# Optimization experiments

Measured on AMD Instinct MI355X. Metric: run time of the kernel, lower is better.

Reference implementation:

```python
import jax, jax.numpy as jnp
import numpy as np
from functools import partial

C = 10   # number of regular-repr fields
G = 4    # C4 rotation group order
EPS = 1e-5


def _lift_kernel(w):
    """Lifting (trivial->regular) P4 kernel. w: [C, Cin, k, k] ->
    full kernel [C*G, Cin, k, k] with output channel layout (field, orientation)."""
    ks = [jnp.rot90(w, r, axes=(-2, -1)) for r in range(G)]  # each [C,Cin,k,k]
    k = jnp.stack(ks, axis=1)                                 # [C,G,Cin,k,k]
    return k.reshape(w.shape[0] * G, w.shape[1], w.shape[2], w.shape[3])


def _gconv_kernel(w):
    """Regular->regular P4 kernel. w: [Cout, Cin, G, k, k] (indexed by relative
    input orientation) -> full kernel [Cout*G, Cin*G, k, k].
    K[co*G+r, ci*G+s] = rot90(w[co, ci, (s-r) mod G], r)."""
    Cout, Cin, _, k1, k2 = w.shape
    ks = []
    for r in range(G):
        wr = jnp.roll(w, shift=r, axis=2)             # wr[..., s, :, :] = w[..., (s-r)%G]
        wr = jnp.rot90(wr, r, axes=(-2, -1))          # rotate spatially by r*90deg
        ks.append(wr)
    k = jnp.stack(ks, axis=1)                          # [Cout, G, Cin, G, k, k]
    return k.reshape(Cout * G, Cin * G, k1, k2)


def _conv(x, k, pad):
    return jax.lax.conv_general_dilated(
        x, k, window_strides=(1, 1), padding=pad,
        dimension_numbers=('NCHW', 'OIHW', 'NCHW'))


def _bn_relu(x, gamma, beta):
    """InnerBatchNorm (stats shared over the G orientations of each field) + ReLU."""
    B, CG, H, W = x.shape
    xr = x.reshape(B, C, G, H, W)
    m = xr.mean(axis=(0, 2, 3, 4), keepdims=True)
    v = xr.var(axis=(0, 2, 3, 4), keepdims=True)
    g = gamma[None, :, None, None, None]
    b = beta[None, :, None, None, None]
    y = (xr - m) * jax.lax.rsqrt(v + EPS) * g + b
    return jnp.maximum(y.reshape(B, CG, H, W), 0.0)


def _maxpool2(x):
    return jax.lax.reduce_window(x, -jnp.inf, jax.lax.max,
                                 (1, 1, 2, 2), (1, 1, 2, 2), 'VALID')


def setup_inputs() -> dict:
    key = jax.random.key(0)
    ks = jax.random.split(key, 20)
    B = 1024
    x = jax.random.normal(ks[0], (B, 1, 28, 28), dtype=jnp.float32)
    w1 = jax.random.normal(ks[1], (C, 1, 3, 3), dtype=jnp.float32) * 0.3
    w2 = jax.random.normal(ks[2], (C, C, G, 3, 3), dtype=jnp.float32) * 0.1
    w3 = jax.random.normal(ks[3], (C, C, G, 3, 3), dtype=jnp.float32) * 0.1
    w4 = jax.random.normal(ks[4], (C, C, G, 3, 3), dtype=jnp.float32) * 0.1
    w5 = jax.random.normal(ks[5], (C, C, G, 3, 3), dtype=jnp.float32) * 0.1
    w6 = jax.random.normal(ks[6], (C, C, G, 3, 3), dtype=jnp.float32) * 0.1
    w7 = jax.random.normal(ks[7], (C, C, G, 4, 4), dtype=jnp.float32) * 0.1
    g1 = jnp.ones((C,), jnp.float32) + 0.1 * jax.random.normal(ks[8], (C,))
    b1 = 0.1 * jax.random.normal(ks[9], (C,))
    g2 = jnp.ones((C,), jnp.float32) + 0.1 * jax.random.normal(ks[10], (C,))
    b2 = 0.1 * jax.random.normal(ks[11], (C,))
    gs = jnp.ones((C,), jnp.float32) + 0.1 * jax.random.normal(ks[12], (C,))
    bs = 0.1 * jax.random.normal(ks[13], (C,))
    wfc = jax.random.normal(ks[14], (10, C * 11 * 11), dtype=jnp.float32) * 0.05
    bfc = jnp.zeros((10,), jnp.float32)
    return dict(x=x, w1=w1, w2=w2, w3=w3, w4=w4, w5=w5, w6=w6, w7=w7,
                g1=g1, b1=b1, g2=g2, b2=b2, gs=gs, bs=bs, wfc=wfc, bfc=bfc)


PAD1 = [(1, 1), (1, 1)]
PAD0 = [(0, 0), (0, 0)]


def reference(x, w1, w2, w3, w4, w5, w6, w7, g1, b1, g2, b2, gs, bs, wfc, bfc):
    # block1: lifting P4 conv 3x3 pad1 + InnerBN + ReLU  -> [B, 40, 28, 28]
    h = _bn_relu(_conv(x, _lift_kernel(w1), PAD1), g1, b1)
    # block2: P4 conv + BN + ReLU + 2x2 max pool         -> [B, 40, 14, 14]
    h = _maxpool2(_bn_relu(_conv(h, _gconv_kernel(w2), PAD1), g2, b2))
    # blocks 3-6: P4 conv + shared BN/ReLU               -> [B, 40, 14, 14]
    for w in (w3, w4, w5, w6):
        h = _bn_relu(_conv(h, _gconv_kernel(w), PAD1), gs, bs)
    # block7: P4 conv 4x4 pad0 + shared BN/ReLU          -> [B, 40, 11, 11]
    h = _bn_relu(_conv(h, _gconv_kernel(w7), PAD0), gs, bs)
    # group pooling: max over the G orientations of each field -> [B, 10, 11, 11]
    B = h.shape[0]
    h = h.reshape(B, C, G, 11, 11).max(axis=2)
    # fc
    return h.reshape(B, -1) @ wfc.T + bfc
```

## Files before the change

### kernel.cpp

```cpp
#include <hip/hip_runtime.h>

#define EPSV 1e-5f
#define INV28 (1.f / 3211264.f)
#define INV14 (1.f / 802816.f)
#define INV11 (1.f / 495616.f)

typedef _Float16 v8h __attribute__((ext_vector_type(8)));
typedef _Float16 v4h __attribute__((ext_vector_type(4)));
typedef float v4f __attribute__((ext_vector_type(4)));

__device__ __forceinline__ int rotsrc(int r, int dy, int dx, int K) {
  int sy, sx;
  if (r == 0)      { sy = dy;       sx = dx; }
  else if (r == 1) { sy = dx;       sx = K - 1 - dy; }
  else if (r == 2) { sy = K - 1 - dy; sx = K - 1 - dx; }
  else             { sy = K - 1 - dx; sx = dy; }
  return sy * K + sx;
}

__device__ __forceinline__ float gw_val(const float* __restrict__ w, int oc, int g,
                                        int j, int KS) {
  int tap = g / 5, cig = g % 5, ci = cig * 8 + j;
  int co = oc >> 2, r = oc & 3, cin = ci >> 2, s = ci & 3;
  int srel = (s - r) & 3;
  return w[((co * 10 + cin) * 4 + srel) * (KS * KS) + rotsrc(r, tap / KS, tap % KS, KS)];
}

__device__ __forceinline__ float stat8a(const float* __restrict__ p, int i) {
  float v = 0.f;
#pragma unroll
  for (int c = 0; c < 8; ++c)
    v += __hip_atomic_load(&p[c * 32 + i], __ATOMIC_RELAXED, __HIP_MEMORY_SCOPE_AGENT);
  return v;
}

__global__ void prep_kernel(const float* __restrict__ w1, const float* __restrict__ w2,
                            const float* __restrict__ w3, const float* __restrict__ w4,
                            const float* __restrict__ w5, const float* __restrict__ w6,
                            const float* __restrict__ w7,
                            float* __restrict__ K1, _Float16* __restrict__ Wb,
                            float* __restrict__ stats) {
  int idx = blockIdx.x * blockDim.x + threadIdx.x;
  if (idx < 1792) { stats[idx] = 0.f; return; }
  idx -= 1792;
  if (idx < 360) {
    int tap = idx / 40, oc = idx % 40;
    int c = oc >> 2, r = oc & 3;
    K1[idx] = w1[c * 9 + rotsrc(r, tap / 3, tap % 3, 3)];
    return;
  }
  idx -= 360;
  if (idx < 92160) {
    int l = idx / 18432, r0 = idx % 18432;
    const float* w = (l == 0) ? w2 : (l == 1) ? w3 : (l == 2) ? w4 : (l == 3) ? w5 : w6;
    int mt = r0 / 6144, r1 = r0 % 6144;
    int c = r1 / 512, r2 = r1 % 512;
    int q = r2 / 128, r3 = r2 % 128;
    int ocl = r3 / 8, j = r3 % 8;
    int oc = mt * 16 + ocl, g = c * 4 + q;
    float val = 0.f;
    if (oc < 40 && g < 45) val = gw_val(w, oc, g, j, 3);
    Wb[idx] = (_Float16)val;
    return;
  }
  idx -= 92160;
  if (idx < 30720) {
    int mt = idx / 10240, r1 = idx % 10240;
    int c = r1 / 512, r2 = r1 % 512;
    int q = r2 / 128, r3 = r2 % 128;
    int ocl = r3 / 8, j = r3 % 8;
    int oc = mt * 16 + ocl, g = c * 4 + q;
    float val = 0.f;
    if (oc < 40) val = gw_val(w7, oc, g, j, 4);
    Wb[92160 + idx] = (_Float16)val;
    return;
  }
  idx -= 30720;
  if (idx < 1536) {
    int mt = idx / 512, r1 = idx % 512;
    int q = r1 / 128, r2 = r1 % 128;
    int ocl = r2 / 8, j = r2 % 8;
    int oc = mt * 16 + ocl, k = q * 8 + j;
    float val = 0.f;
    if (oc < 40 && k < 9)
      val = w1[(oc >> 2) * 9 + rotsrc(oc & 3, k / 3, k % 3, 3)];
    Wb[122880 + idx] = (_Float16)val;
  }
}

__global__ __launch_bounds__(256) void conv1_stats(
    const float* __restrict__ x, const float* __restrict__ K1,
    float* __restrict__ stats) {
  __shared__ float ximg[900];
  __shared__ float wk[360];
  __shared__ float sstat[20];
  const int tid = threadIdx.x, img = blockIdx.x;
  if (tid < 20) sstat[tid] = 0.f;
  for (int i = tid; i < 900; i += 256) {
    int gy = i / 30 - 1, gx = i % 30 - 1;
    ximg[i] = (gy >= 0 && gy < 28 && gx >= 0 && gx < 28)
                  ? x[img * 784 + gy * 28 + gx] : 0.f;
  }
  for (int i = tid; i < 360; i += 256) wk[i] = K1[i];
  __syncthreads();

  float s[10], q[10];
#pragma unroll
  for (int f = 0; f < 10; ++f) { s[f] = 0.f; q[f] = 0.f; }
  for (int p = tid; p < 784; p += 256) {
    const int y = p / 28, xx = p % 28;
    float patch[9];
#pragma unroll
    for (int t = 0; t < 9; ++t) patch[t] = ximg[(y + t / 3) * 30 + xx + t % 3];
#pragma unroll
    for (int f = 0; f < 10; ++f) {
#pragma unroll
      for (int r = 0; r < 4; ++r) {
        const int oc = f * 4 + r;
        float v = 0.f;
#pragma unroll
        for (int t = 0; t < 9; ++t) v = fmaf(patch[t], wk[t * 40 + oc], v);
        s[f] += v; q[f] += v * v;
      }
    }
  }
#pragma unroll
  for (int f = 0; f < 10; ++f) {
#pragma unroll
    for (int off = 1; off <= 32; off <<= 1) {
      s[f] += __shfl_xor(s[f], off, 64);
      q[f] += __shfl_xor(q[f], off, 64);
    }
  }
  if ((tid & 63) == 0) {
#pragma unroll
    for (int f = 0; f < 10; ++f) {
      atomicAdd(&sstat[f], s[f]);
      atomicAdd(&sstat[10 + f], q[f]);
    }
  }
  __syncthreads();
  if (tid < 20) atomicAdd(&stats[(img & 7) * 32 + tid], sstat[tid]);
}

template<int R>
__global__ __launch_bounds__(256) void conv_band_fused(
    const float* __restrict__ x, const _Float16* __restrict__ W1m,
    const _Float16* __restrict__ Wl, const float* __restrict__ pstats,
    const float* __restrict__ pgamma, const float* __restrict__ pbeta,
    float pinvn, _Float16* __restrict__ T0, float* __restrict__ stats) {
  constexpr int NPIX = R * 28, NSUB = NPIX / 16, NSW = (NSUB + 3) / 4;
  constexpr int SROWS = R + 2, XR = R + 4;
  constexpr int NPIX_S = SROWS * 30, NSUB_S = (NPIX_S + 15) / 16;
  __shared__ __attribute__((aligned(16))) _Float16 tile[NPIX_S * 40];
  __shared__ __attribute__((aligned(16))) _Float16 xcol[NPIX_S * 32];
  __shared__ _Float16 xpatch[XR * 32];
  __shared__ float sc[10], sh[10], sstat[20];
  const int tid = threadIdx.x;
  int img, y0;
  if constexpr (R == 8) { img = blockIdx.x / 3; y0 = (blockIdx.x % 3) * 8; }
  else { img = blockIdx.x; y0 = 24; }

  if (tid < 20) sstat[tid] = 0.f;
  if (tid >= 32 && tid < 42) {
    int f = tid - 32;
    float mu = stat8a(pstats, f) * pinvn, q = stat8a(pstats, 10 + f) * pinvn;
    float isd = rsqrtf(q - mu * mu + EPSV);
    float s = pgamma[f] * isd;
    sc[f] = s; sh[f] = pbeta[f] - mu * s;
  }
  for (int i = tid; i < XR * 32; i += 256) {
    int gy = y0 - 2 + i / 32, gx = i % 32 - 2;
    float v = (gy >= 0 && gy < 28 && gx >= 0 && gx < 28)
                  ? x[(long)img * 784 + gy * 28 + gx] : 0.f;
    xpatch[i] = (_Float16)v;
  }
  __syncthreads();

  for (int p = tid; p < NPIX_S; p += 256) {
    const int iy = p / 30, ix = p % 30;
    v8h c0, c1;
#pragma unroll
    for (int j = 0; j < 8; ++j)
      c0[j] = xpatch[(iy + j / 3) * 32 + ix + j % 3];
    c1[0] = xpatch[(iy + 2) * 32 + ix + 2];
#pragma unroll
    for (int j = 1; j < 8; ++j) c1[j] = (_Float16)0.f;
    *(v8h*)&xcol[p * 32] = c0;
    *(v8h*)&xcol[p * 32 + 8] = c1;
    v8h z;
#pragma unroll
    for (int j = 0; j < 8; ++j) z[j] = (_Float16)0.f;
    *(v8h*)&xcol[p * 32 + 16] = z;
    *(v8h*)&xcol[p * 32 + 24] = z;
  }
  __syncthreads();

  const int lane = tid & 63, wv = tid >> 6;
  const int m = lane & 15, quad = lane >> 4;

  {
    v8h a1[3];
#pragma unroll
    for (int mt = 0; mt < 3; ++mt)
      a1[mt] = *(const v8h*)(W1m + mt * 512 + (quad * 16 + m) * 8);
    for (int ns = wv; ns < NSUB_S; ns += 4) {
      const int n = ns * 16 + m;
      const bool valid = n < NPIX_S;
      const int nc = valid ? n : NPIX_S - 1;
      const v8h bfr = *(const v8h*)&xcol[nc * 32 + quad * 8];
      v4f cfr[3];
#pragma unroll
      for (int mt = 0; mt < 3; ++mt)
        cfr[mt] = __builtin_amdgcn_mfma_f32_16x16x32_f16(
            a1[mt], bfr, (v4f){0.f, 0.f, 0.f, 0.f}, 0, 0, 0);
      const int iy = nc / 30, ix = nc % 30;
      const int gy = y0 + iy - 1, gx = ix - 1;
      const bool inb = (gy >= 0 && gy < 28 && gx >= 0 && gx < 28);
#pragma unroll
      for (int mt = 0; mt < 3; ++mt) {
        if (mt == 2 && quad >= 2) continue;
        const int f = mt * 4 + quad;
        const float scf = sc[f], shf = sh[f];
        v4h pk;
#pragma unroll
        for (int r = 0; r < 4; ++r) {
          float v = inb ? fmaxf(0.f, fmaf(cfr[mt][r], scf, shf)) : 0.f;
          pk[r] = (_Float16)v;
        }
        if (valid) *(v4h*)&tile[nc * 40 + mt * 16 + quad * 4] = pk;
      }
    }
  }
  __syncthreads();

  int pbase[NSW], nsv[NSW];
  bool sv[NSW];
#pragma unroll
  for (int s = 0; s < NSW; ++s) {
    int ns = wv + 4 * s;
    sv[s] = ns < NSUB;
    int n = ns * 16 + m;
    n = n < NPIX ? n : NPIX - 1;
    nsv[s] = n;
    pbase[s] = ((n / 28) * 30 + (n % 28)) * 40;
  }
  v4f acc[3][NSW] = {};

  const _Float16* wlane = Wl + (quad * 16 + m) * 8;
  for (int c = 0; c < 12; ++c) {
    int g = 4 * c + quad; g = g > 44 ? 44 : g;
    int tap = g / 5, cig = g - tap * 5;
    int boff = ((tap / 3) * 30 + (tap % 3)) * 40 + cig * 8;
    v8h bfr[NSW];
#pragma unroll
    for (int s = 0; s < NSW; ++s)
      if (sv[s]) bfr[s] = *(const v8h*)&tile[pbase[s] + boff];
    v8h afr[3];
#pragma unroll
    for (int mt = 0; mt < 3; ++mt)
      afr[mt] = *(const v8h*)(wlane + (mt * 12 + c) * 512);
#pragma unroll
    for (int s = 0; s < NSW; ++s)
      if (sv[s]) {
#pragma unroll
        for (int mt = 0; mt < 3; ++mt)
          acc[mt][s] = __builtin_amdgcn_mfma_f32_16x16x32_f16(afr[mt], bfr[s],
                                                             acc[mt][s], 0, 0, 0);
      }
  }

#pragma unroll
  for (int mt = 0; mt < 3; ++mt) {
    float svv = 0.f, qvv = 0.f;
#pragma unroll
    for (int s = 0; s < NSW; ++s)
      if (sv[s]) {
#pragma unroll
        for (int r = 0; r < 4; ++r) { float v = acc[mt][s][r]; svv += v; qvv += v * v; }
      }
    const bool ocok = (mt < 2) || (quad < 2);
#pragma unroll
    for (int off = 1; off <= 8; off <<= 1) {
      svv += __shfl_xor(svv, off, 64);
      qvv += __shfl_xor(qvv, off, 64);
    }
    if (m == 0 && ocok) {
      atomicAdd(&sstat[mt * 4 + quad], svv);
      atomicAdd(&sstat[10 + mt * 4 + quad], qvv);
    }
  }

  __syncthreads();
  _Float16* pool = tile;
#pragma unroll
  for (int mt = 0; mt < 3; ++mt) {
    const bool ocok = (mt < 2) || (quad < 2);
    const int oc0 = mt * 16 + quad * 4;
#pragma unroll
    for (int s = 0; s < NSW; ++s)
      if (ocok && sv[s]) {
#pragma unroll
        for (int r = 0; r < 4; ++r)
          pool[(oc0 + r) * NPIX + nsv[s]] = (_Float16)acc[mt][s][r];
      }
  }
  __syncthreads();
  constexpr int PR = R / 2, PCNT = 40 * PR * 14;
  for (int i = tid; i < PCNT; i += 256) {
    int oc = i / (PR * 14), rem = i % (PR * 14);
    int py = rem / 14, px = rem % 14;
    const _Float16* pp = pool + oc * NPIX + py * 56 + px * 2;
    float a = (float)pp[0], b = (float)pp[1], c = (float)pp[28], d = (float)pp[29];
    T0[((long)img * 256 + (y0 / 2 + py + 1) * 16 + (px + 1)) * 40 + oc] =
        (_Float16)fmaxf(fmaxf(a, b), fmaxf(c, d));
  }
  if (tid < 20) atomicAdd(&stats[(img & 7) * 32 + tid], sstat[tid]);
}

__global__ __launch_bounds__(256) void conv_tile(
    const _Float16* __restrict__ Tin, const _Float16* __restrict__ Wl,
    const float* __restrict__ pstats, const float* __restrict__ pg,
    const float* __restrict__ pb, float pinvn,
    _Float16* __restrict__ Tout, float* __restrict__ stG) {
  __shared__ __attribute__((aligned(16))) _Float16 tile[256 * 40];
  __shared__ float sc[10], sh[10], sstat[20];
  const int tid = threadIdx.x, img = blockIdx.x;
  const int lane = tid & 63, wv = tid >> 6;
  const int m = lane & 15, quad = lane >> 4;
  if (tid < 20) sstat[tid] = 0.f;
  if (tid >= 32 && tid < 42) {
    int f = tid - 32;
    float mu = stat8a(pstats, f) * pinvn, q = stat8a(pstats, 10 + f) * pinvn;
    float isd = rsqrtf(q - mu * mu + EPSV);
    float s = pg[f] * isd;
    sc[f] = s; sh[f] = pb[f] - mu * s;
  }
  __syncthreads();
  {
    const int iy = tid >> 4, ix = tid & 15;
    const bool border = (iy == 0) | (iy == 15) | (ix == 0) | (ix == 15);
    const _Float16* src = Tin + ((long)img * 256 + tid) * 40;
    _Float16* dst = &tile[tid * 40];
#pragma unroll
    for (int cg5 = 0; cg5 < 5; ++cg5) {
      v8h pk;
      if (!border) {
        v8h rv = *(const v8h*)(src + cg5 * 8);
#pragma unroll
        for (int u = 0; u < 8; ++u) {
          const int f = (cg5 * 8 + u) >> 2;
          pk[u] = (_Float16)fmaxf(0.f, fmaf((float)rv[u], sc[f], sh[f]));
        }
      } else {
#pragma unroll
        for (int u = 0; u < 8; ++u) pk[u] = (_Float16)0.f;
      }
      *(v8h*)(dst + cg5 * 8) = pk;
    }
  }
  __syncthreads();

  int pb3[4], n3[4];
  bool sv3[4], va3[4];
#pragma unroll
  for (int s = 0; s < 4; ++s) {
    int ns = wv + 4 * s;
    sv3[s] = ns < 13;
    int n = ns * 16 + m;
    va3[s] = sv3[s] && (n < 196);
    n = n < 196 ? n : 195;
    n3[s] = n;
    pb3[s] = ((n / 14) * 16 + (n % 14)) * 40;
  }
  const int wofs = (quad * 16 + m) * 8;
  v4f acc[3][4];
#pragma unroll
  for (int mt = 0; mt < 3; ++mt)
#pragma unroll
    for (int s = 0; s < 4; ++s) acc[mt][s] = (v4f){0.f, 0.f, 0.f, 0.f};
  for (int c = 0; c < 12; ++c) {
    int g = 4 * c + quad; g = g > 44 ? 44 : g;
    int tap = g / 5, cig = g - tap * 5;
    int boff = ((tap / 3) * 16 + (tap % 3)) * 40 + cig * 8;
    v8h bfr[4];
#pragma unroll
    for (int s = 0; s < 4; ++s)
      if (sv3[s]) bfr[s] = *(const v8h*)&tile[pb3[s] + boff];
    v8h afr[3];
#pragma unroll
    for (int mt = 0; mt < 3; ++mt)
      afr[mt] = *(const v8h*)(Wl + wofs + (mt * 12 + c) * 512);
#pragma unroll
    for (int s = 0; s < 4; ++s)
      if (sv3[s]) {
#pragma unroll
        for (int mt = 0; mt < 3; ++mt)
          acc[mt][s] = __builtin_amdgcn_mfma_f32_16x16x32_f16(afr[mt], bfr[s],
                                                             acc[mt][s], 0, 0, 0);
      }
  }

#pragma unroll
  for (int mt = 0; mt < 3; ++mt) {
    float svv = 0.f, qvv = 0.f;
#pragma unroll
    for (int s = 0; s < 4; ++s)
      if (va3[s]) {
#pragma unroll
        for (int r = 0; r < 4; ++r) { float v = acc[mt][s][r]; svv += v; qvv += v * v; }
      }
    const bool ocok = (mt < 2) || (quad < 2);
#pragma unroll
    for (int off = 1; off <= 8; off <<= 1) {
      svv += __shfl_xor(svv, off, 64);
      qvv += __shfl_xor(qvv, off, 64);
    }
    if (m == 0 && ocok) {
      atomicAdd(&sstat[mt * 4 + quad], svv);
      atomicAdd(&sstat[10 + mt * 4 + quad], qvv);
    }
  }
  __syncthreads();
  if (tid < 20) atomicAdd(&stG[(img & 7) * 32 + tid], sstat[tid]);

#pragma unroll
  for (int mt = 0; mt < 3; ++mt) {
    const bool ocok = (mt < 2) || (quad < 2);
    if (!ocok) continue;
#pragma unroll
    for (int s = 0; s < 4; ++s)
      if (va3[s]) {
        v4h pk;
#pragma unroll
        for (int r = 0; r < 4; ++r) pk[r] = (_Float16)acc[mt][s][r];
        const int n = n3[s];
        *(v4h*)(Tout + ((long)img * 256 + (n / 14 + 1) * 16 + (n % 14 + 1)) * 40
                + mt * 16 + quad * 4) = pk;
      }
  }
}

__global__ __launch_bounds__(256) void conv7_tile(
    const _Float16* __restrict__ Tin, const _Float16* __restrict__ Wl,
    const float* __restrict__ pstats, const float* __restrict__ pg,
    const float* __restrict__ pb,
    _Float16* __restrict__ T7, float* __restrict__ stG) {
  __shared__ __attribute__((aligned(16))) _Float16 tile[256 * 40];
  __shared__ float sc[10], sh[10], sstat[20];
  const int tid = threadIdx.x, img = blockIdx.x;
  const int lane = tid & 63, wv = tid >> 6;
  const int m = lane & 15, quad = lane >> 4;
  if (tid < 20) sstat[tid] = 0.f;
  if (tid >= 32 && tid < 42) {
    int f = tid - 32;
    float mu = stat8a(pstats, f) * INV14, q = stat8a(pstats, 10 + f) * INV14;
    float isd = rsqrtf(q - mu * mu + EPSV);
    float s = pg[f] * isd;
    sc[f] = s; sh[f] = pb[f] - mu * s;
  }
  __syncthreads();
  {
    const int iy = tid >> 4, ix = tid & 15;
    const bool border = (iy == 0) | (iy == 15) | (ix == 0) | (ix == 15);
    const _Float16* src = Tin + ((long)img * 256 + tid) * 40;
    _Float16* dst = &tile[tid * 40];
#pragma unroll
    for (int cg5 = 0; cg5 < 5; ++cg5) {
      v8h pk;
      if (!border) {
        v8h rv = *(const v8h*)(src + cg5 * 8);
#pragma unroll
        for (int u = 0; u < 8; ++u) {
          const int f = (cg5 * 8 + u) >> 2;
          pk[u] = (_Float16)fmaxf(0.f, fmaf((float)rv[u], sc[f], sh[f]));
        }
      } else {
#pragma unroll
        for (int u = 0; u < 8; ++u) pk[u] = (_Float16)0.f;
      }
      *(v8h*)(dst + cg5 * 8) = pk;
    }
  }
  __syncthreads();

  int pb7[2], n7[2];
  bool va7[2];
#pragma unroll
  for (int s = 0; s < 2; ++s) {
    int ns = wv + 4 * s;
    int n = ns * 16 + m;
    va7[s] = n < 121;
    n = n < 121 ? n : 120;
    n7[s] = n;
    pb7[s] = ((n / 11 + 1) * 16 + (n % 11 + 1)) * 40;
  }
  const int wofs = (quad * 16 + m) * 8;
  v4f acc[3][2];
#pragma unroll
  for (int mt = 0; mt < 3; ++mt)
#pragma unroll
    for (int s = 0; s < 2; ++s) acc[mt][s] = (v4f){0.f, 0.f, 0.f, 0.f};
  for (int c = 0; c < 20; ++c) {
    int g = 4 * c + quad;
    int tap = g / 5, cig = g - tap * 5;
    int boff = ((tap >> 2) * 16 + (tap & 3)) * 40 + cig * 8;
    v8h bfr[2];
#pragma unroll
    for (int s = 0; s < 2; ++s) bfr[s] = *(const v8h*)&tile[pb7[s] + boff];
    v8h afr[3];
#pragma unroll
    for (int mt = 0; mt < 3; ++mt)
      afr[mt] = *(const v8h*)(Wl + wofs + (mt * 20 + c) * 512);
#pragma unroll
    for (int s = 0; s < 2; ++s)
#pragma unroll
      for (int mt = 0; mt < 3; ++mt)
        acc[mt][s] = __builtin_amdgcn_mfma_f32_16x16x32_f16(afr[mt], bfr[s],
                                                           acc[mt][s], 0, 0, 0);
  }

#pragma unroll
  for (int mt = 0; mt < 3; ++mt) {
    float svv = 0.f, qvv = 0.f;
#pragma unroll
    for (int s = 0; s < 2; ++s)
      if (va7[s]) {
#pragma unroll
        for (int r = 0; r < 4; ++r) { float v = acc[mt][s][r]; svv += v; qvv += v * v; }
      }
    const bool ocok = (mt < 2) || (quad < 2);
#pragma unroll
    for (int off = 1; off <= 8; off <<= 1) {
      svv += __shfl_xor(svv, off, 64);
      qvv += __shfl_xor(qvv, off, 64);
    }
    if (m == 0 && ocok) {
      atomicAdd(&sstat[mt * 4 + quad], svv);
      atomicAdd(&sstat[10 + mt * 4 + quad], qvv);
    }
  }
  __syncthreads();
  if (tid < 20) atomicAdd(&stG[(img & 7) * 32 + tid], sstat[tid]);

#pragma unroll
  for (int mt = 0; mt < 3; ++mt) {
    const bool ocok = (mt < 2) || (quad < 2);
    if (!ocok) continue;
#pragma unroll
    for (int s = 0; s < 2; ++s)
      if (va7[s]) {
        v4h pk;
#pragma unroll
        for (int r = 0; r < 4; ++r) pk[r] = (_Float16)acc[mt][s][r];
        *(v4h*)(T7 + ((long)img * 121 + n7[s]) * 40 + mt * 16 + quad * 4) = pk;
      }
  }
}

__global__ __launch_bounds__(256) void head_kernel(
    const _Float16* __restrict__ T7, const float* __restrict__ stats7,
    const float* __restrict__ gs, const float* __restrict__ bs,
    const float* __restrict__ wfc, const float* __restrict__ bfc,
    float* __restrict__ out) {
  __shared__ float sc[10], sh[10];
  __shared__ float mbuf[1210];
  __shared__ float red[40];
  const int tid = threadIdx.x, img = blockIdx.x;
  if (tid < 10) {
    float mu = stat8a(stats7, tid) * INV11, q = stat8a(stats7, 10 + tid) * INV11;
    float isd = rsqrtf(q - mu * mu + EPSV);
    float s = gs[tid] * isd;
    sc[tid] = s;
    sh[tid] = bs[tid] - mu * s;
  }
  __syncthreads();
  for (int p = tid; p < 121; p += 256) {
    const _Float16* rp = T7 + ((long)img * 121 + p) * 40;
#pragma unroll
    for (int cg5 = 0; cg5 < 5; ++cg5) {
      v8h v = *(const v8h*)(rp + cg5 * 8);
#pragma unroll
      for (int fh = 0; fh < 2; ++fh) {
        const int f = cg5 * 2 + fh;
        float mx = fmaf((float)v[fh * 4], sc[f], sh[f]);
#pragma unroll
        for (int r = 1; r < 4; ++r)
          mx = fmaxf(mx, fmaf((float)v[fh * 4 + r], sc[f], sh[f]));
        mbuf[f * 121 + p] = fmaxf(0.f, mx);
      }
    }
  }
  __syncthreads();
  const int wv = tid >> 6;
  for (int k = 0; k < 10; ++k) {
    float p = 0.f;
    for (int j = tid; j < 1210; j += 256) p = fmaf(mbuf[j], wfc[k * 1210 + j], p);
#pragma unroll
    for (int off = 32; off > 0; off >>= 1) p += __shfl_xor(p, off, 64);
    if ((tid & 63) == 0) red[k * 4 + wv] = p;
  }
  __syncthreads();
  if (tid < 10)
    out[img * 10 + tid] = bfc[tid] + red[tid * 4] + red[tid * 4 + 1] +
                          red[tid * 4 + 2] + red[tid * 4 + 3];
}

extern "C" void kernel_launch(void* const* d_in, const int* in_sizes, int n_in,
                              void* d_out, int out_size, void* d_ws, size_t ws_size,
                              hipStream_t stream) {
  const float* x   = (const float*)d_in[0];
  const float* w1  = (const float*)d_in[1];
  const float* w2  = (const float*)d_in[2];
  const float* w3  = (const float*)d_in[3];
  const float* w4  = (const float*)d_in[4];
  const float* w5  = (const float*)d_in[5];
  const float* w6  = (const float*)d_in[6];
  const float* w7  = (const float*)d_in[7];
  const float* g1  = (const float*)d_in[8];
  const float* b1  = (const float*)d_in[9];
  const float* g2  = (const float*)d_in[10];
  const float* b2  = (const float*)d_in[11];
  const float* gs  = (const float*)d_in[12];
  const float* bs  = (const float*)d_in[13];
  const float* wfc = (const float*)d_in[14];
  const float* bfc = (const float*)d_in[15];

  float* ws = (float*)d_ws;
  float* K1      = ws;
  float* stats   = ws + 360;
  _Float16* Wb   = (_Float16*)(ws + 2152);
  _Float16* W1m  = Wb + 122880;
  _Float16* T0   = (_Float16*)(ws + 64360);
  _Float16* T1   = (_Float16*)(ws + 5307240L);
  _Float16* T7   = (_Float16*)(ws + 10550120L);

  prep_kernel<<<495, 256, 0, stream>>>(w1, w2, w3, w4, w5, w6, w7, K1, Wb, stats);
  conv1_stats<<<1024, 256, 0, stream>>>(x, K1, stats);
  conv_band_fused<8><<<3072, 256, 0, stream>>>(x, W1m, Wb, stats, g1, b1, INV28,
                                               T0, stats + 256);
  conv_band_fused<4><<<1024, 256, 0, stream>>>(x, W1m, Wb, stats, g1, b1, INV28,
                                               T0, stats + 256);
  conv_tile<<<1024, 256, 0, stream>>>(T0, Wb + 18432, stats + 256, g2, b2, INV28,
                                      T1, stats + 512);
  conv_tile<<<1024, 256, 0, stream>>>(T1, Wb + 36864, stats + 512, gs, bs, INV14,
                                      T0, stats + 768);
  conv_tile<<<1024, 256, 0, stream>>>(T0, Wb + 55296, stats + 768, gs, bs, INV14,
                                      T1, stats + 1024);
  conv_tile<<<1024, 256, 0, stream>>>(T1, Wb + 73728, stats + 1024, gs, bs, INV14,
                                      T0, stats + 1280);
  conv7_tile<<<1024, 256, 0, stream>>>(T0, Wb + 92160, stats + 1280, gs, bs,
                                       T7, stats + 1536);
  head_kernel<<<1024, 256, 0, stream>>>(T7, stats + 1536, gs, bs, wfc, bfc,
                                        (float*)d_out);
}
```

Before: 321.5 us.

## Merge band conv launches and split mid-layer convs into two blocks per image

The two templated band kernels for conv2 are replaced by one runtime-parameterised kernel launched with four blocks per image, and the im2col buffer is shrunk to 16 halves per pixel with zero fragments built in registers. conv_tile and conv7_tile now launch two blocks per image, each covering half the output subtiles. The aim is to cut one launch and to raise parallelism and occupancy by using smaller per-block register and accumulator footprints. The cost is that each half-block reloads and recomputes the full input tile, including BN-ReLU of the halo, and issues double the stats atomics.

```diff
diff --git a/kernel.cpp b/kernel.cpp
--- a/kernel.cpp
+++ b/kernel.cpp
@@ -143,23 +143,23 @@
   if (tid < 20) atomicAdd(&stats[(img & 7) * 32 + tid], sstat[tid]);
 }
 
-template<int R>
-__global__ __launch_bounds__(256) void conv_band_fused(
+__global__ __launch_bounds__(256) void conv_band_all(
     const float* __restrict__ x, const _Float16* __restrict__ W1m,
     const _Float16* __restrict__ Wl, const float* __restrict__ pstats,
     const float* __restrict__ pgamma, const float* __restrict__ pbeta,
     float pinvn, _Float16* __restrict__ T0, float* __restrict__ stats) {
-  constexpr int NPIX = R * 28, NSUB = NPIX / 16, NSW = (NSUB + 3) / 4;
-  constexpr int SROWS = R + 2, XR = R + 4;
-  constexpr int NPIX_S = SROWS * 30, NSUB_S = (NPIX_S + 15) / 16;
-  __shared__ __attribute__((aligned(16))) _Float16 tile[NPIX_S * 40];
-  __shared__ __attribute__((aligned(16))) _Float16 xcol[NPIX_S * 32];
-  __shared__ _Float16 xpatch[XR * 32];
+  __shared__ __attribute__((aligned(16))) _Float16 tile[300 * 40];
+  __shared__ __attribute__((aligned(16))) _Float16 xcol[300 * 16];
+  __shared__ _Float16 xpatch[12 * 32];
   __shared__ float sc[10], sh[10], sstat[20];
   const int tid = threadIdx.x;
-  int img, y0;
-  if constexpr (R == 8) { img = blockIdx.x / 3; y0 = (blockIdx.x % 3) * 8; }
-  else { img = blockIdx.x; y0 = 24; }
+  const int img = blockIdx.x >> 2, slot = blockIdx.x & 3;
+  const int R = (slot < 3) ? 8 : 4;
+  const int y0 = (slot < 3) ? slot * 8 : 24;
+  const int npix = R * 28, nsub = npix >> 4;
+  const int srows = R + 2, npix_s = srows * 30;
+  const int nsub_s = (npix_s + 15) >> 4;
+  const int xr = R + 4;
 
   if (tid < 20) sstat[tid] = 0.f;
   if (tid >= 32 && tid < 42) {
@@ -169,7 +169,7 @@
     float s = pgamma[f] * isd;
     sc[f] = s; sh[f] = pbeta[f] - mu * s;
   }
-  for (int i = tid; i < XR * 32; i += 256) {
+  for (int i = tid; i < xr * 32; i += 256) {
     int gy = y0 - 2 + i / 32, gx = i % 32 - 2;
     float v = (gy >= 0 && gy < 28 && gx >= 0 && gx < 28)
                   ? x[(long)img * 784 + gy * 28 + gx] : 0.f;
@@ -177,7 +177,7 @@
   }
   __syncthreads();
 
-  for (int p = tid; p < NPIX_S; p += 256) {
+  for (int p = tid; p < npix_s; p += 256) {
     const int iy = p / 30, ix = p % 30;
     v8h c0, c1;
 #pragma unroll
@@ -186,13 +186,8 @@
     c1[0] = xpatch[(iy + 2) * 32 + ix + 2];
 #pragma unroll
     for (int j = 1; j < 8; ++j) c1[j] = (_Float16)0.f;
-    *(v8h*)&xcol[p * 32] = c0;
-    *(v8h*)&xcol[p * 32 + 8] = c1;
-    v8h z;
-#pragma unroll
-    for (int j = 0; j < 8; ++j) z[j] = (_Float16)0.f;
-    *(v8h*)&xcol[p * 32 + 16] = z;
-    *(v8h*)&xcol[p * 32 + 24] = z;
+    *(v8h*)&xcol[p * 16] = c0;
+    *(v8h*)&xcol[p * 16 + 8] = c1;
   }
   __syncthreads();
 
@@ -204,11 +199,14 @@
 #pragma unroll
     for (int mt = 0; mt < 3; ++mt)
       a1[mt] = *(const v8h*)(W1m + mt * 512 + (quad * 16 + m) * 8);
-    for (int ns = wv; ns < NSUB_S; ns += 4) {
+    v8h zf;
+#pragma unroll
+    for (int j = 0; j < 8; ++j) zf[j] = (_Float16)0.f;
+    for (int ns = wv; ns < nsub_s; ns += 4) {
       const int n = ns * 16 + m;
-      const bool valid = n < NPIX_S;
-      const int nc = valid ? n : NPIX_S - 1;
-      const v8h bfr = *(const v8h*)&xcol[nc * 32 + quad * 8];
+      const bool valid = n < npix_s;
+      const int nc = valid ? n : npix_s - 1;
+      const v8h bfr = (quad < 2) ? *(const v8h*)&xcol[nc * 16 + quad * 8] : zf;
       v4f cfr[3];
 #pragma unroll
       for (int mt = 0; mt < 3; ++mt)
@@ -234,34 +232,34 @@
   }
   __syncthreads();
 
-  int pbase[NSW], nsv[NSW];
-  bool sv[NSW];
-#pragma unroll
-  for (int s = 0; s < NSW; ++s) {
+  int pbase[4], nsv[4];
+  bool sv[4];
+#pragma unroll
+  for (int s = 0; s < 4; ++s) {
     int ns = wv + 4 * s;
-    sv[s] = ns < NSUB;
+    sv[s] = ns < nsub;
     int n = ns * 16 + m;
-    n = n < NPIX ? n : NPIX - 1;
+    n = n < npix ? n : npix - 1;
     nsv[s] = n;
     pbase[s] = ((n / 28) * 30 + (n % 28)) * 40;
   }
-  v4f acc[3][NSW] = {};
+  v4f acc[3][4] = {};
 
   const _Float16* wlane = Wl + (quad * 16 + m) * 8;
   for (int c = 0; c < 12; ++c) {
     int g = 4 * c + quad; g = g > 44 ? 44 : g;
     int tap = g / 5, cig = g - tap * 5;
     int boff = ((tap / 3) * 30 + (tap % 3)) * 40 + cig * 8;
-    v8h bfr[NSW];
-#pragma unroll
-    for (int s = 0; s < NSW; ++s)
+    v8h bfr[4];
+#pragma unroll
+    for (int s = 0; s < 4; ++s)
       if (sv[s]) bfr[s] = *(const v8h*)&tile[pbase[s] + boff];
     v8h afr[3];
 #pragma unroll
     for (int mt = 0; mt < 3; ++mt)
       afr[mt] = *(const v8h*)(wlane + (mt * 12 + c) * 512);
 #pragma unroll
-    for (int s = 0; s < NSW; ++s)
+    for (int s = 0; s < 4; ++s)
       if (sv[s]) {
 #pragma unroll
         for (int mt = 0; mt < 3; ++mt)
@@ -274,7 +272,7 @@
   for (int mt = 0; mt < 3; ++mt) {
     float svv = 0.f, qvv = 0.f;
 #pragma unroll
-    for (int s = 0; s < NSW; ++s)
+    for (int s = 0; s < 4; ++s)
       if (sv[s]) {
 #pragma unroll
         for (int r = 0; r < 4; ++r) { float v = acc[mt][s][r]; svv += v; qvv += v * v; }
@@ -298,19 +296,19 @@
     const bool ocok = (mt < 2) || (quad < 2);
     const int oc0 = mt * 16 + quad * 4;
 #pragma unroll
-    for (int s = 0; s < NSW; ++s)
+    for (int s = 0; s < 4; ++s)
       if (ocok && sv[s]) {
 #pragma unroll
         for (int r = 0; r < 4; ++r)
-          pool[(oc0 + r) * NPIX + nsv[s]] = (_Float16)acc[mt][s][r];
-      }
-  }
-  __syncthreads();
-  constexpr int PR = R / 2, PCNT = 40 * PR * 14;
-  for (int i = tid; i < PCNT; i += 256) {
-    int oc = i / (PR * 14), rem = i % (PR * 14);
+          pool[(oc0 + r) * npix + nsv[s]] = (_Float16)acc[mt][s][r];
+      }
+  }
+  __syncthreads();
+  const int pr = R / 2, pcnt = 40 * pr * 14;
+  for (int i = tid; i < pcnt; i += 256) {
+    int oc = i / (pr * 14), rem = i % (pr * 14);
     int py = rem / 14, px = rem % 14;
-    const _Float16* pp = pool + oc * NPIX + py * 56 + px * 2;
+    const _Float16* pp = pool + oc * npix + py * 56 + px * 2;
     float a = (float)pp[0], b = (float)pp[1], c = (float)pp[28], d = (float)pp[29];
     T0[((long)img * 256 + (y0 / 2 + py + 1) * 16 + (px + 1)) * 40 + oc] =
         (_Float16)fmaxf(fmaxf(a, b), fmaxf(c, d));
@@ -325,7 +323,8 @@
     _Float16* __restrict__ Tout, float* __restrict__ stG) {
   __shared__ __attribute__((aligned(16))) _Float16 tile[256 * 40];
   __shared__ float sc[10], sh[10], sstat[20];
-  const int tid = threadIdx.x, img = blockIdx.x;
+  const int tid = threadIdx.x;
+  const int img = blockIdx.x >> 1, half = blockIdx.x & 1;
   const int lane = tid & 63, wv = tid >> 6;
   const int m = lane & 15, quad = lane >> 4;
   if (tid < 20) sstat[tid] = 0.f;
@@ -361,11 +360,11 @@
   }
   __syncthreads();
 
-  int pb3[4], n3[4];
-  bool sv3[4], va3[4];
-#pragma unroll
-  for (int s = 0; s < 4; ++s) {
-    int ns = wv + 4 * s;
+  int pb3[2], n3[2];
+  bool sv3[2], va3[2];
+#pragma unroll
+  for (int s = 0; s < 2; ++s) {
+    int ns = wv + 4 * (2 * half + s);
     sv3[s] = ns < 13;
     int n = ns * 16 + m;
     va3[s] = sv3[s] && (n < 196);
@@ -374,25 +373,25 @@
     pb3[s] = ((n / 14) * 16 + (n % 14)) * 40;
   }
   const int wofs = (quad * 16 + m) * 8;
-  v4f acc[3][4];
+  v4f acc[3][2];
 #pragma unroll
   for (int mt = 0; mt < 3; ++mt)
 #pragma unroll
-    for (int s = 0; s < 4; ++s) acc[mt][s] = (v4f){0.f, 0.f, 0.f, 0.f};
+    for (int s = 0; s < 2; ++s) acc[mt][s] = (v4f){0.f, 0.f, 0.f, 0.f};
   for (int c = 0; c < 12; ++c) {
     int g = 4 * c + quad; g = g > 44 ? 44 : g;
     int tap = g / 5, cig = g - tap * 5;
     int boff = ((tap / 3) * 16 + (tap % 3)) * 40 + cig * 8;
-    v8h bfr[4];
-#pragma unroll
-    for (int s = 0; s < 4; ++s)
+    v8h bfr[2];
+#pragma unroll
+    for (int s = 0; s < 2; ++s)
       if (sv3[s]) bfr[s] = *(const v8h*)&tile[pb3[s] + boff];
     v8h afr[3];
 #pragma unroll
     for (int mt = 0; mt < 3; ++mt)
       afr[mt] = *(const v8h*)(Wl + wofs + (mt * 12 + c) * 512);
 #pragma unroll
-    for (int s = 0; s < 4; ++s)
+    for (int s = 0; s < 2; ++s)
       if (sv3[s]) {
 #pragma unroll
         for (int mt = 0; mt < 3; ++mt)
@@ -405,7 +404,7 @@
   for (int mt = 0; mt < 3; ++mt) {
     float svv = 0.f, qvv = 0.f;
 #pragma unroll
-    for (int s = 0; s < 4; ++s)
+    for (int s = 0; s < 2; ++s)
       if (va3[s]) {
 #pragma unroll
         for (int r = 0; r < 4; ++r) { float v = acc[mt][s][r]; svv += v; qvv += v * v; }
@@ -429,7 +428,7 @@
     const bool ocok = (mt < 2) || (quad < 2);
     if (!ocok) continue;
 #pragma unroll
-    for (int s = 0; s < 4; ++s)
+    for (int s = 0; s < 2; ++s)
       if (va3[s]) {
         v4h pk;
 #pragma unroll
@@ -448,7 +447,8 @@
     _Float16* __restrict__ T7, float* __restrict__ stG) {
   __shared__ __attribute__((aligned(16))) _Float16 tile[256 * 40];
   __shared__ float sc[10], sh[10], sstat[20];
-  const int tid = threadIdx.x, img = blockIdx.x;
+  const int tid = threadIdx.x;
+  const int img = blockIdx.x >> 1, half = blockIdx.x & 1;
   const int lane = tid & 63, wv = tid >> 6;
   const int m = lane & 15, quad = lane >> 4;
   if (tid < 20) sstat[tid] = 0.f;
@@ -484,51 +484,37 @@
   }
   __syncthreads();
 
-  int pb7[2], n7[2];
-  bool va7[2];
-#pragma unroll
-  for (int s = 0; s < 2; ++s) {
-    int ns = wv + 4 * s;
-    int n = ns * 16 + m;
-    va7[s] = n < 121;
-    n = n < 121 ? n : 120;
-    n7[s] = n;
-    pb7[s] = ((n / 11 + 1) * 16 + (n % 11 + 1)) * 40;
-  }
+  const int ns = wv + 4 * half;
+  const int n0 = ns * 16 + m;
+  const bool va = n0 < 121;
+  const int n7 = va ? n0 : 120;
+  const int pb7 = ((n7 / 11 + 1) * 16 + (n7 % 11 + 1)) * 40;
   const int wofs = (quad * 16 + m) * 8;
-  v4f acc[3][2];
-#pragma unroll
-  for (int mt = 0; mt < 3; ++mt)
-#pragma unroll
-    for (int s = 0; s < 2; ++s) acc[mt][s] = (v4f){0.f, 0.f, 0.f, 0.f};
+  v4f acc[3];
+#pragma unroll
+  for (int mt = 0; mt < 3; ++mt) acc[mt] = (v4f){0.f, 0.f, 0.f, 0.f};
   for (int c = 0; c < 20; ++c) {
     int g = 4 * c + quad;
     int tap = g / 5, cig = g - tap * 5;
     int boff = ((tap >> 2) * 16 + (tap & 3)) * 40 + cig * 8;
-    v8h bfr[2];
-#pragma unroll
-    for (int s = 0; s < 2; ++s) bfr[s] = *(const v8h*)&tile[pb7[s] + boff];
+    const v8h bfr = *(const v8h*)&tile[pb7 + boff];
     v8h afr[3];
 #pragma unroll
     for (int mt = 0; mt < 3; ++mt)
       afr[mt] = *(const v8h*)(Wl + wofs + (mt * 20 + c) * 512);
 #pragma unroll
-    for (int s = 0; s < 2; ++s)
-#pragma unroll
-      for (int mt = 0; mt < 3; ++mt)
-        acc[mt][s] = __builtin_amdgcn_mfma_f32_16x16x32_f16(afr[mt], bfr[s],
-                                                           acc[mt][s], 0, 0, 0);
+    for (int mt = 0; mt < 3; ++mt)
+      acc[mt] = __builtin_amdgcn_mfma_f32_16x16x32_f16(afr[mt], bfr, acc[mt],
+                                                       0, 0, 0);
   }
 
 #pragma unroll
   for (int mt = 0; mt < 3; ++mt) {
     float svv = 0.f, qvv = 0.f;
-#pragma unroll
-    for (int s = 0; s < 2; ++s)
-      if (va7[s]) {
-#pragma unroll
-        for (int r = 0; r < 4; ++r) { float v = acc[mt][s][r]; svv += v; qvv += v * v; }
-      }
+    if (va) {
+#pragma unroll
+      for (int r = 0; r < 4; ++r) { float v = acc[mt][r]; svv += v; qvv += v * v; }
+    }
     const bool ocok = (mt < 2) || (quad < 2);
 #pragma unroll
     for (int off = 1; off <= 8; off <<= 1) {
@@ -547,14 +533,12 @@
   for (int mt = 0; mt < 3; ++mt) {
     const bool ocok = (mt < 2) || (quad < 2);
     if (!ocok) continue;
-#pragma unroll
-    for (int s = 0; s < 2; ++s)
-      if (va7[s]) {
-        v4h pk;
-#pragma unroll
-        for (int r = 0; r < 4; ++r) pk[r] = (_Float16)acc[mt][s][r];
-        *(v4h*)(T7 + ((long)img * 121 + n7[s]) * 40 + mt * 16 + quad * 4) = pk;
-      }
+    if (va) {
+      v4h pk;
+#pragma unroll
+      for (int r = 0; r < 4; ++r) pk[r] = (_Float16)acc[mt][r];
+      *(v4h*)(T7 + ((long)img * 121 + n7) * 40 + mt * 16 + quad * 4) = pk;
+    }
   }
 }
 
@@ -637,19 +621,17 @@
 
   prep_kernel<<<495, 256, 0, stream>>>(w1, w2, w3, w4, w5, w6, w7, K1, Wb, stats);
   conv1_stats<<<1024, 256, 0, stream>>>(x, K1, stats);
-  conv_band_fused<8><<<3072, 256, 0, stream>>>(x, W1m, Wb, stats, g1, b1, INV28,
-                                               T0, stats + 256);
-  conv_band_fused<4><<<1024, 256, 0, stream>>>(x, W1m, Wb, stats, g1, b1, INV28,
-                                               T0, stats + 256);
-  conv_tile<<<1024, 256, 0, stream>>>(T0, Wb + 18432, stats + 256, g2, b2, INV28,
+  conv_band_all<<<4096, 256, 0, stream>>>(x, W1m, Wb, stats, g1, b1, INV28,
+                                          T0, stats + 256);
+  conv_tile<<<2048, 256, 0, stream>>>(T0, Wb + 18432, stats + 256, g2, b2, INV28,
                                       T1, stats + 512);
-  conv_tile<<<1024, 256, 0, stream>>>(T1, Wb + 36864, stats + 512, gs, bs, INV14,
+  conv_tile<<<2048, 256, 0, stream>>>(T1, Wb + 36864, stats + 512, gs, bs, INV14,
                                       T0, stats + 768);
-  conv_tile<<<1024, 256, 0, stream>>>(T0, Wb + 55296, stats + 768, gs, bs, INV14,
+  conv_tile<<<2048, 256, 0, stream>>>(T0, Wb + 55296, stats + 768, gs, bs, INV14,
                                       T1, stats + 1024);
-  conv_tile<<<1024, 256, 0, stream>>>(T1, Wb + 73728, stats + 1024, gs, bs, INV14,
+  conv_tile<<<2048, 256, 0, stream>>>(T1, Wb + 73728, stats + 1024, gs, bs, INV14,
                                       T0, stats + 1280);
-  conv7_tile<<<1024, 256, 0, stream>>>(T0, Wb + 92160, stats + 1280, gs, bs,
+  conv7_tile<<<2048, 256, 0, stream>>>(T0, Wb + 92160, stats + 1280, gs, bs,
                                        T7, stats + 1536);
   head_kernel<<<1024, 256, 0, stream>>>(T7, stats + 1536, gs, bs, wfc, bfc,
                                         (float*)d_out);
```

Measured after the change: 358.4 us. +11.5%, slower.
